# Kernel optimization log

Hardware: AMD Instinct MI355X
Metric: run time of the kernel (lower is better)

Reference implementation:

```python
import jax, jax.numpy as jnp
import numpy as np

SLOT_DIM = 256
HIDDEN = 128
NUM_REL = 8


def setup_inputs() -> dict:
    key = jax.random.key(0)
    ks = jax.random.split(key, 5)
    B, N, D = 8, 256, SLOT_DIM
    slots = jax.random.normal(ks[0], (B, N, D), dtype=jnp.float32)
    # Linear(2D -> H): store as [2D, H] (x @ W + b)
    s1 = 1.0 / np.sqrt(2 * D)
    W1 = jax.random.uniform(ks[1], (2 * D, HIDDEN), jnp.float32, -s1, s1)
    b1 = jax.random.uniform(ks[2], (HIDDEN,), jnp.float32, -s1, s1)
    s2 = 1.0 / np.sqrt(HIDDEN)
    W2 = jax.random.uniform(ks[3], (HIDDEN, NUM_REL), jnp.float32, -s2, s2)
    b2 = jax.random.uniform(ks[4], (NUM_REL,), jnp.float32, -s2, s2)
    return {"slots": slots, "W1": W1, "b1": b1, "W2": W2, "b2": b2}


def reference(slots, W1, b1, W2, b2):
    # cat([slots_i, slots_j]) @ W1 == slots_i @ W1[:D] + slots_j @ W1[D:]
    # so project each slot once, then broadcast-add over the pair grid.
    D = slots.shape[-1]
    proj_i = jnp.einsum("bnd,dh->bnh", slots, W1[:D])   # [B,N,H]
    proj_j = jnp.einsum("bnd,dh->bnh", slots, W1[D:])   # [B,N,H]
    h = proj_i[:, :, None, :] + proj_j[:, None, :, :] + b1  # [B,N,N,H]
    h = jax.nn.relu(h)
    logits = jnp.einsum("bijh,hr->bijr", h, W2) + b2     # [B,N,N,R]
    return jax.nn.sigmoid(logits)
```

## Files before the change

kernel.cpp:

```cpp
#include <hip/hip_runtime.h>
#include <hip/hip_fp16.h>
#include <math.h>

#define BATCH 8
#define NSLOT 256
#define DDIM  256
#define HID   128
#define NREL  8

typedef _Float16 half8 __attribute__((ext_vector_type(8)));
typedef float float4v __attribute__((ext_vector_type(4)));

union U8 {
  uint32_t u[4];
  _Float16 f[8];
  half8 v;
  float4 f4;
};

__global__ __launch_bounds__(256, 4) void proj_kernel(
    const float* __restrict__ slots, const float* __restrict__ W1,
    const float* __restrict__ b1, _Float16* __restrict__ P) {
  const int tid  = threadIdx.x;
  const int row0 = blockIdx.x * 2;
  const int c    = tid;
  const bool isP1 = (c < HID);
  const float* Wcol = isP1 ? (W1 + c) : (W1 + DDIM * HID + (c - HID));
  const float bias = isP1 ? b1[c] : 0.0f;

  float acc0 = bias, acc1 = bias;
  const float* srow = slots + (size_t)row0 * DDIM;

  for (int k = 0; k < DDIM; k += 16) {
    float w[16];
#pragma unroll
    for (int u = 0; u < 16; ++u) w[u] = Wcol[(size_t)(k + u) * HID];
#pragma unroll
    for (int u = 0; u < 16; ++u) {
      acc0 = fmaf(srow[k + u], w[u], acc0);
      acc1 = fmaf(srow[DDIM + k + u], w[u], acc1);
    }
  }

  P[(size_t)(row0)     * 256 + c] = (_Float16)acc0;
  P[(size_t)(row0 + 1) * 256 + c] = (_Float16)acc1;
}

__global__ __launch_bounds__(256) void pair_kernel(
    const _Float16* __restrict__ P, const float* __restrict__ W2,
    const float* __restrict__ b2, float* __restrict__ out) {
  __shared__ uint32_t PiL[16 * 68];

  const int tid  = threadIdx.x;
  const int w    = tid >> 6;
  const int lane = tid & 63;
  const int n    = lane & 15;
  const int kg   = lane >> 4;

  const int b   = blockIdx.z;
  const int i0  = blockIdx.y * 16;
  const int j0  = blockIdx.x * 64 + w * 16;
  const _Float16* Pb = P + (size_t)b * NSLOT * 256;

  {
    const int r  = tid >> 4;
    const int ch = tid & 15;
    const float4 t = *(const float4*)(Pb + (size_t)(i0 + r) * 256 + ch * 8);
    *(float4*)&PiL[r * 68 + ch * 4] = t;
  }
  __syncthreads();

  U8 w2f[4];
#pragma unroll
  for (int kq = 0; kq < 4; ++kq) {
#pragma unroll
    for (int u = 0; u < 8; ++u) {
      const int k = kq * 32 + kg * 8 + u;
      w2f[kq].f[u] = (n < 8) ? (_Float16)W2[k * NREL + n] : (_Float16)0.0f;
    }
  }
  const float b2v = (n < 8) ? b2[n] : 0.0f;

  U8 pj[4];
#pragma unroll
  for (int kq = 0; kq < 4; ++kq) {
    pj[kq].f4 = *(const float4*)(Pb + (size_t)(j0 + n) * 256 + HID + kq * 32 + kg * 8);
  }

  for (int i = 0; i < 16; ++i) {
    float4v acc = {0.0f, 0.0f, 0.0f, 0.0f};
#pragma unroll
    for (int kq = 0; kq < 4; ++kq) {
      U8 pi;
      pi.f4 = *(const float4*)&PiL[i * 68 + kq * 16 + kg * 4];
      U8 h;
      h.v = __builtin_elementwise_max(pj[kq].v + pi.v, (half8)(_Float16)0.0f);
      acc = __builtin_amdgcn_mfma_f32_16x16x32_f16(h.v, w2f[kq].v, acc, 0, 0, 0);
    }
    if (n < 8) {
      float* obase = out + (((size_t)b * NSLOT + (i0 + i)) * NSLOT + j0) * NREL + n;
#pragma unroll
      for (int reg = 0; reg < 4; ++reg) {
        const int jrow = kg * 4 + reg;
        const float x = acc[reg] + b2v;
        obase[jrow * NREL] = __builtin_amdgcn_rcpf(1.0f + __expf(-x));
      }
    }
  }
}

extern "C" void kernel_launch(void* const* d_in, const int* in_sizes, int n_in,
                              void* d_out, int out_size, void* d_ws, size_t ws_size,
                              hipStream_t stream) {
  const float* slots = (const float*)d_in[0];
  const float* W1    = (const float*)d_in[1];
  const float* b1    = (const float*)d_in[2];
  const float* W2    = (const float*)d_in[3];
  const float* b2    = (const float*)d_in[4];
  float* out    = (float*)d_out;
  _Float16* P   = (_Float16*)d_ws;

  proj_kernel<<<dim3(BATCH * NSLOT / 2), 256, 0, stream>>>(slots, W1, b1, P);
  pair_kernel<<<dim3(NSLOT / 64, NSLOT / 16, BATCH), 256, 0, stream>>>(P, W2, b2, out);
}
```

Measured before the change: 86.51 us.

## Compute slot projection with MFMA using a pre-transposed fp16 weight copy

```diff
diff --git a/kernel.cpp b/kernel.cpp
--- a/kernel.cpp
+++ b/kernel.cpp
@@ -18,32 +18,89 @@
   float4 f4;
 };
 
-__global__ __launch_bounds__(256, 4) void proj_kernel(
-    const float* __restrict__ slots, const float* __restrict__ W1,
+union H4 {
+  _Float16 f[4];
+  double d;
+};
+
+
+__global__ __launch_bounds__(256) void wt_kernel(
+    const float* __restrict__ W1, _Float16* __restrict__ WT) {
+  __shared__ float T[32][33];
+  const int tx = threadIdx.x & 31;
+  const int ty = threadIdx.x >> 5;
+  const int c0 = blockIdx.x * 32, k0 = blockIdx.y * 32;
+#pragma unroll
+  for (int p = 0; p < 4; ++p) {
+    const int k = k0 + ty + p * 8;
+    const int c = c0 + tx;
+    T[ty + p * 8][tx] = (c < HID) ? W1[(size_t)k * HID + c]
+                                  : W1[(size_t)(DDIM + k) * HID + (c - HID)];
+  }
+  __syncthreads();
+#pragma unroll
+  for (int p = 0; p < 4; ++p) {
+    const int cl = ty + p * 8;
+    WT[(size_t)(c0 + cl) * 256 + k0 + tx] = (_Float16)T[tx][cl];
+  }
+}
+
+__global__ __launch_bounds__(128) void proj_kernel(
+    const float* __restrict__ slots, const _Float16* __restrict__ WT,
     const float* __restrict__ b1, _Float16* __restrict__ P) {
+  __shared__ _Float16 SL[16 * 264];
+
   const int tid  = threadIdx.x;
-  const int row0 = blockIdx.x * 2;
-  const int c    = tid;
-  const bool isP1 = (c < HID);
-  const float* Wcol = isP1 ? (W1 + c) : (W1 + DDIM * HID + (c - HID));
-  const float bias = isP1 ? b1[c] : 0.0f;
+  const int w    = tid >> 6;
+  const int lane = tid & 63;
+  const int lo16 = lane & 15;
+  const int kg   = lane >> 4;
+  const int row0 = blockIdx.y * 16;
+  const int c0   = blockIdx.x * 64 + w * 32;
 
-  float acc0 = bias, acc1 = bias;
-  const float* srow = slots + (size_t)row0 * DDIM;
+  U8 bf[2][8];
+#pragma unroll
+  for (int t = 0; t < 2; ++t)
+#pragma unroll
+    for (int ks = 0; ks < 8; ++ks)
+      bf[t][ks].f4 =
+          *(const float4*)(WT + (size_t)(c0 + t * 16 + lo16) * 256 + ks * 32 + kg * 8);
 
-  for (int k = 0; k < DDIM; k += 16) {
-    float w[16];
+  const float* S0 = slots + (size_t)row0 * DDIM;
 #pragma unroll
-    for (int u = 0; u < 16; ++u) w[u] = Wcol[(size_t)(k + u) * HID];
+  for (int p = 0; p < 8; ++p) {
+    const int idx = tid + p * 128;
+    const int r  = idx >> 6;
+    const int c4 = (idx & 63) * 4;
+    const float4 f = *(const float4*)(S0 + (size_t)r * DDIM + c4);
+    H4 h;
+    h.f[0] = (_Float16)f.x; h.f[1] = (_Float16)f.y;
+    h.f[2] = (_Float16)f.z; h.f[3] = (_Float16)f.w;
+    *(double*)&SL[r * 264 + c4] = h.d;
+  }
+  __syncthreads();
+
+  float4v acc0 = {0.0f, 0.0f, 0.0f, 0.0f};
+  float4v acc1 = {0.0f, 0.0f, 0.0f, 0.0f};
 #pragma unroll
-    for (int u = 0; u < 16; ++u) {
-      acc0 = fmaf(srow[k + u], w[u], acc0);
-      acc1 = fmaf(srow[DDIM + k + u], w[u], acc1);
+  for (int ks = 0; ks < 8; ++ks) {
+    U8 a;
+    a.f4 = *(const float4*)&SL[lo16 * 264 + ks * 32 + kg * 8];
+    acc0 = __builtin_amdgcn_mfma_f32_16x16x32_f16(a.v, bf[0][ks].v, acc0, 0, 0, 0);
+    acc1 = __builtin_amdgcn_mfma_f32_16x16x32_f16(a.v, bf[1][ks].v, acc1, 0, 0, 0);
+  }
+
+#pragma unroll
+  for (int t = 0; t < 2; ++t) {
+    const int cg = c0 + t * 16 + lo16;
+    const float bias = (cg < HID) ? b1[cg] : 0.0f;
+    const float4v& A = t ? acc1 : acc0;
+#pragma unroll
+    for (int reg = 0; reg < 4; ++reg) {
+      const int row = row0 + kg * 4 + reg;
+      P[(size_t)row * 256 + cg] = (_Float16)(A[reg] + bias);
     }
   }
-
-  P[(size_t)(row0)     * 256 + c] = (_Float16)acc0;
-  P[(size_t)(row0 + 1) * 256 + c] = (_Float16)acc1;
 }
 
 __global__ __launch_bounds__(256) void pair_kernel(
@@ -117,9 +174,11 @@
   const float* b1    = (const float*)d_in[2];
   const float* W2    = (const float*)d_in[3];
   const float* b2    = (const float*)d_in[4];
-  float* out    = (float*)d_out;
-  _Float16* P   = (_Float16*)d_ws;
+  float* out     = (float*)d_out;
+  _Float16* WT   = (_Float16*)d_ws;
+  _Float16* P    = (_Float16*)((char*)d_ws + (1 << 20));
 
-  proj_kernel<<<dim3(BATCH * NSLOT / 2), 256, 0, stream>>>(slots, W1, b1, P);
+  wt_kernel  <<<dim3(8, 8),            256, 0, stream>>>(W1, WT);
+  proj_kernel<<<dim3(4, 128),          128, 0, stream>>>(slots, WT, b1, P);
   pair_kernel<<<dim3(NSLOT / 64, NSLOT / 16, BATCH), 256, 0, stream>>>(P, W2, b2, out);
 }
```

Measured after the change: 108.9 us. 1.26x slower.
